# Optimization experiments

Measured on AMD Instinct MI355X. Metric: run time of the kernel, lower is better.

The kernel has to match this reference:

```python
import jax, jax.numpy as jnp
import numpy as np

B, C, H, W = 8, 256, 128, 128
P = 7          # patch_size (odd)
N = 500        # n_infer (eval mode)
HIDDEN = C // 16  # reduction=16


def setup_inputs() -> dict:
    key = jax.random.key(0)
    ks = jax.random.split(key, 8)
    def s(k, shape, fan_in):
        return jax.random.normal(k, shape, jnp.float32) * (1.0 / np.sqrt(fan_in))
    return {
        "x_main": jax.random.normal(ks[0], (B, C, H, W), jnp.float32),
        "x_aux": jax.random.normal(ks[1], (B, C, H, W), jnp.float32),
        "scorer_w": s(ks[2], (C,), C),            # 1x1 conv C->1
        "scorer_b": s(ks[3], (1,), C),
        "fc1_w": s(ks[4], (3 * C, HIDDEN), 3 * C),
        "fc1_b": jnp.zeros((HIDDEN,), jnp.float32),
        "fc2_w": s(ks[5], (HIDDEN, C), HIDDEN),
        "fc2_b": jnp.zeros((C,), jnp.float32),
        "proj_w": s(ks[6], (C, C), C),
        "proj_b": jnp.zeros((C,), jnp.float32),
        "n": N,
    }


def _sample_patch_feats(feat, px, py):
    # feat: [C,H,W]; px,py: [n,p,p] pixel coords (align_corners=False convention).
    # Bilinear sample with zero padding, then pool 0.5*(mean+max) over the patch.
    c, h, w = feat.shape
    x0 = jnp.floor(px); y0 = jnp.floor(py)
    wx1 = px - x0; wy1 = py - y0
    def gather(yi, xi):
        valid = ((yi >= 0) & (yi < h) & (xi >= 0) & (xi < w)).astype(feat.dtype)
        yc = jnp.clip(yi, 0, h - 1).astype(jnp.int32)
        xc = jnp.clip(xi, 0, w - 1).astype(jnp.int32)
        return feat[:, yc, xc] * valid  # [C,n,p,p]
    patch = (gather(y0, x0) * ((1 - wy1) * (1 - wx1))
             + gather(y0, x0 + 1) * ((1 - wy1) * wx1)
             + gather(y0 + 1, x0) * (wy1 * (1 - wx1))
             + gather(y0 + 1, x0 + 1) * (wy1 * wx1))  # [C,n,p,p]
    v = 0.5 * (patch.mean(axis=(2, 3)) + patch.max(axis=(2, 3)))  # [C,n]
    return v.T  # [n,C]


def reference(x_main, x_aux, scorer_w, scorer_b, fc1_w, fc1_b, fc2_w, fc2_b, proj_w, proj_b, n):
    b, c, h, w = x_main.shape
    # saliency scores -> topk indices over flattened HW
    score = jax.nn.sigmoid(jnp.einsum('bchw,c->bhw', x_main, scorer_w) + scorer_b[0])
    score = score.reshape(b, h * w)
    _, idx = jax.lax.top_k(score, n)  # [b,n] int32
    idx_y = idx // w
    idx_x = idx - idx_y * w
    # build the (clamped) normalized grid exactly as the torch module does,
    # then convert to pixel coords: px = ((g+1)*W - 1)/2 (align_corners=False)
    r = P // 2
    d = jnp.arange(-r, r + 1, dtype=jnp.float32)
    yy, xx = jnp.meshgrid(d, d, indexing='ij')
    off_x = xx * (2.0 / w); off_y = yy * (2.0 / h)           # [p,p]
    cx = (idx_x.astype(jnp.float32) + 0.5) * (2.0 / w) - 1.0  # [b,n]
    cy = (idx_y.astype(jnp.float32) + 0.5) * (2.0 / h) - 1.0
    gx = jnp.clip(cx[:, :, None, None] + off_x, -1.0, 1.0)    # [b,n,p,p]
    gy = jnp.clip(cy[:, :, None, None] + off_y, -1.0, 1.0)
    px = ((gx + 1.0) * w - 1.0) * 0.5
    py = ((gy + 1.0) * h - 1.0) * 0.5
    sample = jax.vmap(_sample_patch_feats)
    v_main = sample(x_main, px, py)  # [b,n,C]
    v_aux = sample(x_aux, px, py)    # aux_in_proj is Identity (c_main==c_aux)
    # instance-level cross attention
    sim = jnp.einsum('bnc,bmc->bnm', v_main, v_aux) / jnp.sqrt(jnp.float32(c))
    attn = jax.nn.softmax(sim, axis=-1)
    v_hat = jnp.einsum('bnm,bmc->bnc', attn, v_aux)
    # gated fusion MLP
    z = jnp.concatenate([v_main, v_hat, v_main - v_hat], axis=-1)  # [b,n,3C]
    gate = jax.nn.sigmoid(jax.nn.relu(z @ fc1_w + fc1_b) @ fc2_w + fc2_b)
    v_fused = v_main + gate * (v_main - v_hat)
    v_inj = v_fused @ proj_w + proj_b  # [b,n,C]
    # scatter-add reinjection at the topk locations
    inject = jnp.zeros((b, h * w, c), x_main.dtype)
    inject = inject.at[jnp.arange(b)[:, None], idx].add(v_inj)
    inject = inject.reshape(b, h, w, c).transpose(0, 3, 1, 2)
    return x_main + inject
```

## Files before the change

### kernel.cpp

```cpp
#include <hip/hip_runtime.h>
#include <cstdint>
#include <cstddef>

#define HW    16384
#define CCH   256
#define WID   128
#define NB    8
#define NSEL  500
#define NPAD  512
#define CPG   16

__device__ __forceinline__ unsigned key_of(float f) {
  unsigned u = __float_as_uint(f);
  return (u & 0x80000000u) ? ~u : (u | 0x80000000u);
}

__global__ __launch_bounds__(256) void score_copy_kernel(const float* __restrict__ x,
                                                         const float* __restrict__ w,
                                                         float* __restrict__ logits,
                                                         float* __restrict__ out) {
  __shared__ float ws[CCH];
  int tid = threadIdx.x;
  ws[tid] = w[tid];
  __syncthreads();
  int pix = blockIdx.x * 256 + tid;
  int b = pix >> 14, p = pix & (HW - 1);
  const float* xp = x + ((size_t)b << 22) + p;
  float* op = out + ((size_t)b << 22) + p;
  float acc = 0.f;
#pragma unroll 8
  for (int c = 0; c < CCH; c++) {
    float v = xp[(size_t)c * HW];
    acc += v * ws[c];
    __builtin_nontemporal_store(v, &op[(size_t)c * HW]);
  }
  logits[pix] = acc;
}

__global__ __launch_bounds__(1024) void topk_kernel(const float* __restrict__ logits,
                                                    int* __restrict__ idx_out) {
  int b = blockIdx.x, tid = threadIdx.x;
  int lane = tid & 63, wave = tid >> 6;
  const float* lg = logits + (size_t)b * HW;
  __shared__ unsigned hist[256];
  __shared__ unsigned wtot[4];
  __shared__ unsigned wsum[16];
  __shared__ unsigned bc_prefix;
  __shared__ int bc_want;
  __shared__ int cnt;

  unsigned kreg[16];
#pragma unroll
  for (int j = 0; j < 4; j++) {
    float4 v = *(const float4*)&lg[tid * 16 + j * 4];
    kreg[4 * j + 0] = key_of(v.x);
    kreg[4 * j + 1] = key_of(v.y);
    kreg[4 * j + 2] = key_of(v.z);
    kreg[4 * j + 3] = key_of(v.w);
  }

  unsigned prefix = 0;
  int want = NSEL;
  for (int shift = 24; shift >= 0; shift -= 8) {
    if (tid < 256) hist[tid] = 0;
    __syncthreads();
#pragma unroll
    for (int j = 0; j < 16; j++) {
      unsigned u = kreg[j];
      bool m = (shift == 24) || ((u >> (shift + 8)) == (prefix >> (shift + 8)));
      if (m) atomicAdd(&hist[(u >> shift) & 255u], 1u);
    }
    __syncthreads();
    unsigned h = (tid < 256) ? hist[tid] : 0u;
    unsigned v = h;
#pragma unroll
    for (int o = 1; o < 64; o <<= 1) {
      unsigned t = __shfl_down(v, o);
      if (lane < 64 - o) v += t;
    }
    if (tid < 256 && lane == 0) wtot[wave] = v;
    __syncthreads();
    if (tid < 256) {
      unsigned sfx = v;
      for (int w2 = wave + 1; w2 < 4; w2++) sfx += wtot[w2];
      unsigned above = sfx - h;
      if ((int)sfx >= want && (int)above < want) {
        bc_prefix = prefix | ((unsigned)tid << shift);
        bc_want = want - (int)above;
      }
    }
    __syncthreads();
    prefix = bc_prefix;
    want = bc_want;
  }
  unsigned thr = prefix;

  int local = 0;
#pragma unroll
  for (int j = 0; j < 16; j++) local += (kreg[j] == thr) ? 1 : 0;
  unsigned pv = (unsigned)local;
#pragma unroll
  for (int o = 1; o < 64; o <<= 1) {
    unsigned t = __shfl_up(pv, o);
    if (lane >= o) pv += t;
  }
  if (lane == 63) wsum[wave] = pv;
  if (tid == 0) cnt = 0;
  __syncthreads();
  unsigned woff = 0;
  for (int w2 = 0; w2 < wave; w2++) woff += wsum[w2];
  int rank = (int)(woff + pv) - local;
#pragma unroll
  for (int j = 0; j < 16; j++) {
    unsigned u = kreg[j];
    bool take = (u > thr);
    if (u == thr) { if (rank < want) take = true; rank++; }
    if (take) {
      int s = atomicAdd(&cnt, 1);
      idx_out[b * NPAD + s] = tid * 16 + j;
    }
  }
}

__device__ __forceinline__ void patch_weights(int p, int* xc, int* yc, float* wx, float* wy) {
  int iy = p >> 7, ix = p & (WID - 1);
#pragma unroll
  for (int d = 0; d < 7; d++) {
    int t = ix + d - 3;
    bool in = (t >= 0) && (t < WID);
    xc[d] = in ? t : (t < 0 ? 0 : WID - 1);
    wx[d] = in ? 1.f : 0.5f;
    t = iy + d - 3;
    in = (t >= 0) && (t < WID);
    yc[d] = in ? t : (t < 0 ? 0 : WID - 1);
    wy[d] = in ? 1.f : 0.5f;
  }
}

__global__ __launch_bounds__(512) void gather_dma_kernel(const float* __restrict__ xm,
                                                         const float* __restrict__ xa,
                                                         const int* __restrict__ idx,
                                                         float* __restrict__ vmainT,
                                                         float* __restrict__ vauxT) {
  extern __shared__ float plane2[];
  int g = blockIdx.x, b = blockIdx.y, z = blockIdx.z;
  int tid = threadIdx.x;
  int c0 = g * CPG;
  const float* src = (z == 0 ? xm : xa) + ((size_t)(b * CCH + c0)) * HW;
  float* dst = (z == 0 ? vmainT : vauxT) + (((size_t)(b * CCH + c0)) << 9);

  int t500 = (tid < NSEL) ? tid : 0;
  int p = idx[b * NPAD + t500];
  float wx[7], wy[7];
  int xc[7], yc[7], rb[7];
  patch_weights(p, xc, yc, wx, wy);
#pragma unroll
  for (int d = 0; d < 7; d++) rb[d] = yc[d] * WID;

#pragma unroll
  for (int j = 0; j < 8; j++) {
    int off = (tid + j * 512) * 4;
    __builtin_amdgcn_global_load_lds(
        (const __attribute__((address_space(1))) float*)(src + off),
        (__attribute__((address_space(3))) float*)(plane2 + off), 16, 0, 0);
  }
  __syncthreads();

  for (int c = 0; c < CPG; c++) {
    float* cur = plane2 + ((c & 1) ? HW : 0);
    float* nxt = plane2 + ((c & 1) ? 0 : HW);
    if (c + 1 < CPG) {
      const float* s2 = src + (size_t)(c + 1) * HW;
#pragma unroll
      for (int j = 0; j < 8; j++) {
        int off = (tid + j * 512) * 4;
        __builtin_amdgcn_global_load_lds(
            (const __attribute__((address_space(1))) float*)(s2 + off),
            (__attribute__((address_space(3))) float*)(nxt + off), 16, 0, 0);
      }
    }
    if (tid < NSEL) {
      float s = 0.f, mx = -INFINITY;
#pragma unroll
      for (int dy = 0; dy < 7; dy++) {
        float rs = 0.f, rm = -INFINITY;
        int rbb = rb[dy];
        float wyd = wy[dy];
#pragma unroll
        for (int dx = 0; dx < 7; dx++) {
          float v = cur[rbb + xc[dx]] * wx[dx];
          rs += v;
          rm = fmaxf(rm, v);
        }
        s += rs * wyd;
        mx = fmaxf(mx, rm * wyd);
      }
      dst[((size_t)c << 9) + tid] = 0.5f * (s * (1.f / 49.f) + mx);
    } else {
      dst[((size_t)c << 9) + tid] = 0.f;
    }
    __syncthreads();
  }
}

template <int M, int N, int K, bool AT, bool BT, bool BSHARED, int EPI>
__global__ __launch_bounds__(256) void gemm_kernel(const float* __restrict__ A,
                                                   const float* __restrict__ B,
                                                   float* __restrict__ C,
                                                   const float* __restrict__ bias) {
  constexpr int BM = 64, BN = 64, BK = 16;
  __shared__ float As[BK][BM + 4];
  __shared__ float Bs[BK][BN + 4];
  int tid = threadIdx.x;
  int bx = blockIdx.x, by = blockIdx.y, b = blockIdx.z;
  const float* Ab = A + (size_t)b * M * K;
  const float* Bb = BSHARED ? B : (B + (size_t)b * ((size_t)K * N));
  int tx = tid & 15, ty = tid >> 4;
  float acc[4][4] = {};

  for (int k0 = 0; k0 < K; k0 += BK) {
    if (!AT) {
      int ar = tid >> 2, ac4 = (tid & 3) * 4;
      const float4 av = *(const float4*)&Ab[(size_t)(by * BM + ar) * K + k0 + ac4];
      As[ac4 + 0][ar] = av.x; As[ac4 + 1][ar] = av.y;
      As[ac4 + 2][ar] = av.z; As[ac4 + 3][ar] = av.w;
    } else {
      int kr = tid >> 4, mc = (tid & 15) * 4;
      *(float4*)&As[kr][mc] = *(const float4*)&Ab[(size_t)(k0 + kr) * M + by * BM + mc];
    }
    if (!BT) {
      int br = tid >> 4, bc4 = (tid & 15) * 4;
      *(float4*)&Bs[br][bc4] = *(const float4*)&Bb[(size_t)(k0 + br) * N + bx * BN + bc4];
    } else {
      int nr = tid >> 2, kc4 = (tid & 3) * 4;
      const float4 bv = *(const float4*)&Bb[(size_t)(bx * BN + nr) * K + k0 + kc4];
      Bs[kc4 + 0][nr] = bv.x; Bs[kc4 + 1][nr] = bv.y;
      Bs[kc4 + 2][nr] = bv.z; Bs[kc4 + 3][nr] = bv.w;
    }
    __syncthreads();
#pragma unroll
    for (int kk = 0; kk < BK; kk++) {
      const float4 a = *(const float4*)&As[kk][ty * 4];
      const float4 bb = *(const float4*)&Bs[kk][tx * 4];
      float av[4] = {a.x, a.y, a.z, a.w};
      float bv[4] = {bb.x, bb.y, bb.z, bb.w};
#pragma unroll
      for (int rr = 0; rr < 4; rr++)
#pragma unroll
        for (int ss = 0; ss < 4; ss++) acc[rr][ss] += av[rr] * bv[ss];
    }
    __syncthreads();
  }
  if (EPI == 2) {
#pragma unroll
    for (int s = 0; s < 4; s++) {
      int col = bx * BN + tx * 4 + s;
      float bv = bias[col];
#pragma unroll
      for (int r = 0; r < 4; r++) {
        int row = by * BM + ty * 4 + r;
        C[((size_t)b * N + col) * M + row] = acc[r][s] + bv;
      }
    }
  } else {
    float scale = (EPI == 1) ? 0.0625f : 1.f;
#pragma unroll
    for (int r = 0; r < 4; r++) {
      int row = by * BM + ty * 4 + r;
#pragma unroll
      for (int s = 0; s < 4; s++) {
        int col = bx * BN + tx * 4 + s;
        C[((size_t)b * M + row) * N + col] = acc[r][s] * scale;
      }
    }
  }
}

__global__ __launch_bounds__(256) void softmax_kernel(float* __restrict__ sim) {
  int i = blockIdx.x, b = blockIdx.y, tid = threadIdx.x;
  float* row = sim + ((size_t)b * NPAD + i) * NPAD;
  float v0 = (tid < NSEL) ? row[tid] : -INFINITY;
  int j1 = tid + 256;
  float v1 = (j1 < NSEL) ? row[j1] : -INFINITY;
  float m = fmaxf(v0, v1);
  for (int o = 32; o; o >>= 1) m = fmaxf(m, __shfl_down(m, o));
  __shared__ float red[4];
  __shared__ float bm, bs;
  int wave = tid >> 6, lane = tid & 63;
  if (lane == 0) red[wave] = m;
  __syncthreads();
  if (tid == 0) bm = fmaxf(fmaxf(red[0], red[1]), fmaxf(red[2], red[3]));
  __syncthreads();
  m = bm;
  float e0 = (tid < NSEL) ? expf(v0 - m) : 0.f;
  float e1 = (j1 < NSEL) ? expf(v1 - m) : 0.f;
  float s = e0 + e1;
  for (int o = 32; o; o >>= 1) s += __shfl_down(s, o);
  if (lane == 0) red[wave] = s;
  __syncthreads();
  if (tid == 0) bs = 1.f / (red[0] + red[1] + red[2] + red[3]);
  __syncthreads();
  row[tid] = e0 * bs;
  row[j1] = e1 * bs;
}

__global__ __launch_bounds__(256) void mlp_kernel(const float* __restrict__ vmainT,
                                                  const float* __restrict__ vhat,
                                                  const float* __restrict__ fc1w,
                                                  const float* __restrict__ fc1b,
                                                  const float* __restrict__ fc2w,
                                                  const float* __restrict__ fc2b,
                                                  float* __restrict__ vfused) {
  int i = blockIdx.x, b = blockIdx.y, c = threadIdx.x;
  size_t base = ((size_t)b * NPAD + i) * CCH + c;
  float vm = vmainT[(((size_t)(b * CCH + c)) << 9) + i];
  float vh = vhat[base], vd = vm - vh;
  const float* w0 = fc1w + (size_t)c * 16;
  const float* w1 = fc1w + (size_t)(256 + c) * 16;
  const float* w2 = fc1w + (size_t)(512 + c) * 16;
  __shared__ float ph[256][17];
  __shared__ float part2[16][17];
  __shared__ float hsh[16];
#pragma unroll
  for (int k = 0; k < 16; k++) ph[c][k] = vm * w0[k] + vh * w1[k] + vd * w2[k];
  __syncthreads();
  int kk = c & 15, g = c >> 4;
  float part = 0.f;
#pragma unroll
  for (int j = 0; j < 16; j++) part += ph[g * 16 + j][kk];
  part2[g][kk] = part;
  __syncthreads();
  if (c < 16) {
    float s = fc1b[c];
#pragma unroll
    for (int g2 = 0; g2 < 16; g2++) s += part2[g2][c];
    hsh[c] = fmaxf(s, 0.f);
  }
  __syncthreads();
  float gte = fc2b[c];
#pragma unroll
  for (int k = 0; k < 16; k++) gte += hsh[k] * fc2w[k * 256 + c];
  gte = 1.f / (1.f + expf(-gte));
  vfused[base] = vm + gte * vd;
}

__global__ __launch_bounds__(256) void scatter_kernel(const int* __restrict__ idx,
                                                      const float* __restrict__ vinjT,
                                                      float* __restrict__ out) {
  int c = blockIdx.x, b = blockIdx.y, t = threadIdx.x;
  float* op = out + ((size_t)(b * CCH + c) << 14);
  const float* vp = vinjT + ((size_t)(b * CCH + c) << 9);
  const int* ib = idx + b * NPAD;
  op[ib[t]] += vp[t];
  int s = t + 256;
  if (s < NSEL) op[ib[s]] += vp[s];
}

extern "C" void kernel_launch(void* const* d_in, const int* in_sizes, int n_in,
                              void* d_out, int out_size, void* d_ws, size_t ws_size,
                              hipStream_t stream) {
  const float* x_main   = (const float*)d_in[0];
  const float* x_aux    = (const float*)d_in[1];
  const float* scorer_w = (const float*)d_in[2];
  const float* fc1_w = (const float*)d_in[4];
  const float* fc1_b = (const float*)d_in[5];
  const float* fc2_w = (const float*)d_in[6];
  const float* fc2_b = (const float*)d_in[7];
  const float* proj_w = (const float*)d_in[8];
  const float* proj_b = (const float*)d_in[9];
  (void)in_sizes; (void)n_in; (void)out_size; (void)ws_size;

  float* ws = (float*)d_ws;
  float* logits = ws;
  int*   idx    = (int*)(ws + 131072);
  float* vmainT = ws + 266240;
  float* vauxT  = ws + 1314816;
  float* vhat   = ws + 2363392;
  float* vfused = ws + 3411968;
  float* sim    = ws + 4460544;
  float* vinjT  = vhat;
  float* out = (float*)d_out;

  score_copy_kernel<<<512, 256, 0, stream>>>(x_main, scorer_w, logits, out);
  topk_kernel<<<NB, 1024, 0, stream>>>(logits, idx);
  gather_dma_kernel<<<dim3(CCH / CPG, NB, 2), 512, 2 * HW * sizeof(float), stream>>>(
      x_main, x_aux, idx, vmainT, vauxT);
  gemm_kernel<NPAD, NPAD, CCH, true, false, false, 1>
      <<<dim3(8, 8, NB), 256, 0, stream>>>(vmainT, vauxT, sim, nullptr);
  softmax_kernel<<<dim3(NPAD, NB), 256, 0, stream>>>(sim);
  gemm_kernel<NPAD, CCH, NPAD, false, true, false, 0>
      <<<dim3(4, 8, NB), 256, 0, stream>>>(sim, vauxT, vhat, nullptr);
  mlp_kernel<<<dim3(NPAD, NB), 256, 0, stream>>>(vmainT, vhat, fc1_w, fc1_b,
                                                 fc2_w, fc2_b, vfused);
  gemm_kernel<NPAD, CCH, CCH, false, false, true, 2>
      <<<dim3(4, 8, NB), 256, 0, stream>>>(vfused, proj_w, vinjT, proj_b);
  scatter_kernel<<<dim3(CCH, NB), 256, 0, stream>>>(idx, vinjT, out);
}
```

Before: 490.9 us.

## Prefetch GEMM tiles into registers, privatize topk histograms, unroll score loop more

The GEMM kernel now loads the next K-tile from global memory into registers while computing on the current shared-memory tile, so global load latency overlaps with FMA work. The top-k radix select gives each wave its own 256-bin shared histogram and sums them afterwards, which reduces contention on shared-memory atomics. The channel loop in the score/copy kernel is unrolled 32 instead of 8 so more loads are in flight. The costs are extra registers in the GEMM and score kernels, and 16 KB of shared memory plus a 16-way reduction per radix pass in top-k.

```diff
diff --git a/kernel.cpp b/kernel.cpp
--- a/kernel.cpp
+++ b/kernel.cpp
@@ -28,7 +28,7 @@
   const float* xp = x + ((size_t)b << 22) + p;
   float* op = out + ((size_t)b << 22) + p;
   float acc = 0.f;
-#pragma unroll 8
+#pragma unroll 32
   for (int c = 0; c < CCH; c++) {
     float v = xp[(size_t)c * HW];
     acc += v * ws[c];
@@ -42,7 +42,7 @@
   int b = blockIdx.x, tid = threadIdx.x;
   int lane = tid & 63, wave = tid >> 6;
   const float* lg = logits + (size_t)b * HW;
-  __shared__ unsigned hist[256];
+  __shared__ unsigned histp[16 * 256];
   __shared__ unsigned wtot[4];
   __shared__ unsigned wsum[16];
   __shared__ unsigned bc_prefix;
@@ -62,16 +62,22 @@
   unsigned prefix = 0;
   int want = NSEL;
   for (int shift = 24; shift >= 0; shift -= 8) {
-    if (tid < 256) hist[tid] = 0;
-    __syncthreads();
+#pragma unroll
+    for (int q = 0; q < 4; q++) histp[tid + q * 1024] = 0;
+    __syncthreads();
+    unsigned* myhist = histp + wave * 256;
 #pragma unroll
     for (int j = 0; j < 16; j++) {
       unsigned u = kreg[j];
       bool m = (shift == 24) || ((u >> (shift + 8)) == (prefix >> (shift + 8)));
-      if (m) atomicAdd(&hist[(u >> shift) & 255u], 1u);
-    }
-    __syncthreads();
-    unsigned h = (tid < 256) ? hist[tid] : 0u;
+      if (m) atomicAdd(&myhist[(u >> shift) & 255u], 1u);
+    }
+    __syncthreads();
+    unsigned h = 0;
+    if (tid < 256) {
+#pragma unroll
+      for (int w2 = 0; w2 < 16; w2++) h += histp[w2 * 256 + tid];
+    }
     unsigned v = h;
 #pragma unroll
     for (int o = 1; o < 64; o <<= 1) {
@@ -217,27 +223,36 @@
   const float* Bb = BSHARED ? B : (B + (size_t)b * ((size_t)K * N));
   int tx = tid & 15, ty = tid >> 4;
   float acc[4][4] = {};
-
+  int ar = tid >> 2, ac4 = (tid & 3) * 4;
+  int kr = tid >> 4, mc = (tid & 15) * 4;
+  int br = tid >> 4, bc4 = (tid & 15) * 4;
+  int nr = tid >> 2, kc4 = (tid & 3) * 4;
+
+  auto loadA = [&](int k0) -> float4 {
+    if (!AT) return *(const float4*)&Ab[(size_t)(by * BM + ar) * K + k0 + ac4];
+    else     return *(const float4*)&Ab[(size_t)(k0 + kr) * M + by * BM + mc];
+  };
+  auto loadB = [&](int k0) -> float4 {
+    if (!BT) return *(const float4*)&Bb[(size_t)(k0 + br) * N + bx * BN + bc4];
+    else     return *(const float4*)&Bb[(size_t)(bx * BN + nr) * K + k0 + kc4];
+  };
+
+  float4 avr = loadA(0), bvr = loadB(0);
   for (int k0 = 0; k0 < K; k0 += BK) {
     if (!AT) {
-      int ar = tid >> 2, ac4 = (tid & 3) * 4;
-      const float4 av = *(const float4*)&Ab[(size_t)(by * BM + ar) * K + k0 + ac4];
-      As[ac4 + 0][ar] = av.x; As[ac4 + 1][ar] = av.y;
-      As[ac4 + 2][ar] = av.z; As[ac4 + 3][ar] = av.w;
+      As[ac4 + 0][ar] = avr.x; As[ac4 + 1][ar] = avr.y;
+      As[ac4 + 2][ar] = avr.z; As[ac4 + 3][ar] = avr.w;
     } else {
-      int kr = tid >> 4, mc = (tid & 15) * 4;
-      *(float4*)&As[kr][mc] = *(const float4*)&Ab[(size_t)(k0 + kr) * M + by * BM + mc];
+      *(float4*)&As[kr][mc] = avr;
     }
     if (!BT) {
-      int br = tid >> 4, bc4 = (tid & 15) * 4;
-      *(float4*)&Bs[br][bc4] = *(const float4*)&Bb[(size_t)(k0 + br) * N + bx * BN + bc4];
+      *(float4*)&Bs[br][bc4] = bvr;
     } else {
-      int nr = tid >> 2, kc4 = (tid & 3) * 4;
-      const float4 bv = *(const float4*)&Bb[(size_t)(bx * BN + nr) * K + k0 + kc4];
-      Bs[kc4 + 0][nr] = bv.x; Bs[kc4 + 1][nr] = bv.y;
-      Bs[kc4 + 2][nr] = bv.z; Bs[kc4 + 3][nr] = bv.w;
-    }
-    __syncthreads();
+      Bs[kc4 + 0][nr] = bvr.x; Bs[kc4 + 1][nr] = bvr.y;
+      Bs[kc4 + 2][nr] = bvr.z; Bs[kc4 + 3][nr] = bvr.w;
+    }
+    __syncthreads();
+    if (k0 + BK < K) { avr = loadA(k0 + BK); bvr = loadB(k0 + BK); }
 #pragma unroll
     for (int kk = 0; kk < BK; kk++) {
       const float4 a = *(const float4*)&As[kk][ty * 4];
```

Result: no change. 486.6 us (-0.9%).
